# Optimization experiments

Measured on AMD Instinct MI355X. Metric: run time of the kernel, lower is better.

The kernel has to match this reference:

```python
import jax, jax.numpy as jnp
import numpy as np

S, B, H, V, U = 200, 1024, 128, 100000, 10000
LAMBDA_T = 0.1
LAMBDA_S = 1000.0
DAY = 86400.0


def setup_inputs() -> dict:
    key = jax.random.key(0)
    ks = jax.random.split(key, 14)
    x = jax.random.randint(ks[0], (S, B), 0, V)
    # monotone timestamps per sequence (gaps up to 1 hour)
    gaps = jax.random.uniform(ks[1], (S, B), minval=0.0, maxval=3600.0)
    t = jnp.cumsum(gaps, axis=0).astype(jnp.float32)
    # small spatial extent so exp(-1000*dist) doesn't fully underflow
    s = (jax.random.uniform(ks[2], (S, B, 2)) * 0.01).astype(jnp.float32)
    y_t = jax.random.uniform(ks[3], (S, B), dtype=jnp.float32)
    y_s = jax.random.uniform(ks[4], (S, B, 2), dtype=jnp.float32)
    h = jnp.zeros((B, H), dtype=jnp.float32)
    active_user = jax.random.randint(ks[5], (B,), 0, U)
    length = jax.random.randint(ks[6], (B,), 1, S + 1)
    W_enc = jax.random.normal(ks[7], (V, H), dtype=jnp.float32) * 0.02
    W_user = jax.random.normal(ks[8], (U, H), dtype=jnp.float32) * 0.02
    W_ih = jax.random.normal(ks[9], (H, H), dtype=jnp.float32) * 0.05
    W_hh = jax.random.normal(ks[10], (H, H), dtype=jnp.float32) * 0.05
    b_ih = jnp.zeros((H,), dtype=jnp.float32)
    b_hh = jnp.zeros((H,), dtype=jnp.float32)
    W_fc = jax.random.normal(ks[11], (V, 2 * H), dtype=jnp.float32) * 0.02
    b_fc = jnp.zeros((V,), dtype=jnp.float32)
    return {"x": x, "t": t, "s": s, "y_t": y_t, "y_s": y_s, "h": h,
            "active_user": active_user, "length": length,
            "W_enc": W_enc, "W_user": W_user, "W_ih": W_ih, "W_hh": W_hh,
            "b_ih": b_ih, "b_hh": b_hh, "W_fc": W_fc, "b_fc": b_fc}


def f_t(dt):
    return ((jnp.cos(dt * (2.0 * np.pi / DAY)) + 1.0) * 0.5) * jnp.exp(-(dt / DAY) * LAMBDA_T)


def f_s(ds):
    return jnp.exp(-ds * LAMBDA_S)


def reference(x, t, s, y_t, y_s, h, active_user, length,
              W_enc, W_user, W_ih, W_hh, b_ih, b_hh, W_fc, b_fc):
    seq_len, batch = x.shape
    x_emb = W_enc[x]  # [S,B,H]

    # vanilla tanh RNN over time (packing only affects padded steps, which are masked out below)
    def step(h_prev, x_t):
        h_new = jnp.tanh(x_t @ W_ih.T + b_ih + h_prev @ W_hh.T + b_hh)
        return h_new, h_new
    _, out = jax.lax.scan(step, h, x_emb)      # [S,B,H]
    out = out.transpose(1, 0, 2)               # [B,S,H]

    bidx = jnp.arange(batch)
    last = length - 1
    t_bt = t.T                                 # [B,S]
    s_bt = s.transpose(1, 0, 2)                # [B,S,2]
    t_last = t_bt[bidx, last]                  # [B]
    s_last = s_bt[bidx, last]                  # [B,2]

    dist_t = t_last[:, None] - t_bt                              # [B,S]
    dist_s = jnp.linalg.norm(s_last[:, None, :] - s_bt, axis=-1)  # [B,S]

    mask = jnp.arange(seq_len)[None, :] < length[:, None]        # [B,S] ragged mask
    w = jnp.where(mask, f_t(dist_t) * f_s(dist_s) + 1e-10, 0.0)  # [B,S]

    out_w = jnp.einsum('bs,bsh->bh', w, out) / jnp.sum(w, axis=1, keepdims=True)  # [B,H]

    p_u = W_user[active_user]                  # [B,H]
    out_pu = jnp.concatenate([out_w, p_u], axis=1)  # [B,2H]
    return out_pu @ W_fc.T + b_fc              # [B,V]
```

## Files before the change

kernel.cpp:

```cpp
#include <hip/hip_runtime.h>
#include <stdint.h>

#define S_LEN 200
#define BATCH 1024
#define HID   128
#define VOCAB 100000

typedef __attribute__((ext_vector_type(4))) float f32x4;
typedef __attribute__((ext_vector_type(8))) short bf16x8;

__device__ __forceinline__ unsigned short f2bf(float f) {
  union { float f; uint32_t u; } v; v.f = f;
  uint32_t u = v.u;
  uint32_t r = u + 0x7fffu + ((u >> 16) & 1u);
  return (unsigned short)(r >> 16);
}

__global__ __launch_bounds__(256) void k1_eprecomp(
    const float* __restrict__ Wenc, const float* __restrict__ Wih,
    const float* __restrict__ bih, const float* __restrict__ bhh,
    float* __restrict__ E) {
  __shared__ float Wlds[128][132];
  __shared__ float Alds[64][132];
  const int tid = threadIdx.x;
  const int v0 = blockIdx.x * 64;

  #pragma unroll
  for (int i = 0; i < 16; ++i) {
    int g = tid + i * 256;
    int row = g >> 5, c4 = g & 31;
    *(f32x4*)&Wlds[row][c4 * 4] = *(const f32x4*)&Wih[row * 128 + c4 * 4];
  }
  #pragma unroll
  for (int i = 0; i < 8; ++i) {
    int g = tid + i * 256;
    int row = g >> 5, c4 = g & 31;
    int v = v0 + row;
    *(f32x4*)&Alds[row][c4 * 4] =
        *(const f32x4*)&Wenc[(size_t)(v < VOCAB ? v : 0) * 128 + c4 * 4];
  }
  __syncthreads();

  const int jt = tid & 15, vt = tid >> 4;
  float acc[4][8];
  #pragma unroll
  for (int a = 0; a < 4; ++a)
    #pragma unroll
    for (int b = 0; b < 8; ++b) acc[a][b] = 0.f;

  for (int kk = 0; kk < 32; ++kk) {
    f32x4 av[4], wv[8];
    #pragma unroll
    for (int vv = 0; vv < 4; ++vv) av[vv] = *(const f32x4*)&Alds[vt + 16 * vv][kk * 4];
    #pragma unroll
    for (int jj = 0; jj < 8; ++jj) wv[jj] = *(const f32x4*)&Wlds[jt + 16 * jj][kk * 4];
    #pragma unroll
    for (int vv = 0; vv < 4; ++vv)
      #pragma unroll
      for (int jj = 0; jj < 8; ++jj)
        acc[vv][jj] += av[vv].x * wv[jj].x + av[vv].y * wv[jj].y +
                       av[vv].z * wv[jj].z + av[vv].w * wv[jj].w;
  }

  #pragma unroll
  for (int jj = 0; jj < 8; ++jj) {
    int j = jt + 16 * jj;
    float bias = bih[j] + bhh[j];
    #pragma unroll
    for (int vv = 0; vv < 4; ++vv) {
      int v = v0 + vt + 16 * vv;
      if (v < VOCAB) E[(size_t)v * 128 + j] = acc[vv][jj] + bias;
    }
  }
}

__global__ __launch_bounds__(256) void k1b_weights(
    const float* __restrict__ t, const float* __restrict__ s,
    const int* __restrict__ length, float* __restrict__ wbuf) {
  int idx = blockIdx.x * 256 + threadIdx.x;
  int ts = idx >> 10, b = idx & 1023;
  int len = length[b];
  float w = 0.f;
  if (ts < len) {
    int last = len - 1;
    float tl  = t[last * BATCH + b];
    float slx = s[(last * BATCH + b) * 2 + 0];
    float sly = s[(last * BATCH + b) * 2 + 1];
    float dt = tl - t[ts * BATCH + b];
    float dx = slx - s[(ts * BATCH + b) * 2 + 0];
    float dy = sly - s[(ts * BATCH + b) * 2 + 1];
    float ds = sqrtf(dx * dx + dy * dy);
    float ft = (__cosf(dt * 7.2722052166430399e-05f) + 1.f) * 0.5f *
               __expf(dt * -1.1574074074074073e-06f);
    float fs = __expf(-1000.f * ds);
    w = ft * fs + 1e-10f;
  }
  wbuf[idx] = w;
}

__global__ __launch_bounds__(256) void k2_rnn(
    const int* __restrict__ x, const float* __restrict__ E,
    const float* __restrict__ Whh, const float* __restrict__ h0,
    const float* __restrict__ wbuf,
    const int* __restrict__ active_user, const float* __restrict__ Wuser,
    float* __restrict__ A) {
  __shared__ float hlds[2][2][128];
  const int tid = threadIdx.x;
  const int lane = tid & 63, wv = tid >> 6;
  const int j = wv * 32 + (lane >> 1);
  const int kh = lane & 1;
  const int b0 = blockIdx.x * 2, b1 = b0 + 1;

  f32x4 Wr[16];
  const float* wrow = &Whh[j * 128 + kh * 64];
  #pragma unroll
  for (int i = 0; i < 16; ++i) Wr[i] = *(const f32x4*)&wrow[i * 4];

  { int bb = tid >> 7, jj = tid & 127;
    hlds[0][bb][jj] = h0[(b0 + bb) * 128 + jj]; }
  __syncthreads();

  float acc0 = 0.f, acc1 = 0.f, ws0 = 0.f, ws1 = 0.f;
  int xc0 = x[b0], xc1 = x[b1];
  int xn0 = x[1024 + b0], xn1 = x[1024 + b1];
  float ec0 = E[(size_t)xc0 * 128 + j], ec1 = E[(size_t)xc1 * 128 + j];
  float wc0 = wbuf[b0], wc1 = wbuf[b1];

  for (int t = 0; t < S_LEN; ++t) {
    int rb = t & 1, wb = rb ^ 1;
    int xf0 = 0, xf1 = 0;
    float en0 = 0.f, en1 = 0.f, wn0 = 0.f, wn1 = 0.f;
    if (t + 2 < S_LEN) { xf0 = x[(t + 2) * 1024 + b0]; xf1 = x[(t + 2) * 1024 + b1]; }
    if (t + 1 < S_LEN) {
      en0 = E[(size_t)xn0 * 128 + j]; en1 = E[(size_t)xn1 * 128 + j];
      wn0 = wbuf[(t + 1) * 1024 + b0]; wn1 = wbuf[(t + 1) * 1024 + b1];
    }
    float p0 = 0.f, p1 = 0.f;
    const float* h0p = &hlds[rb][0][kh * 64];
    const float* h1p = &hlds[rb][1][kh * 64];
    #pragma unroll
    for (int i = 0; i < 16; ++i) {
      f32x4 hv0 = *(const f32x4*)&h0p[i * 4];
      f32x4 hv1 = *(const f32x4*)&h1p[i * 4];
      p0 += Wr[i].x * hv0.x + Wr[i].y * hv0.y + Wr[i].z * hv0.z + Wr[i].w * hv0.w;
      p1 += Wr[i].x * hv1.x + Wr[i].y * hv1.y + Wr[i].z * hv1.z + Wr[i].w * hv1.w;
    }
    p0 += __shfl_xor(p0, 1, 64);
    p1 += __shfl_xor(p1, 1, 64);
    float hn0 = tanhf(p0 + ec0);
    float hn1 = tanhf(p1 + ec1);
    acc0 += wc0 * hn0; ws0 += wc0;
    acc1 += wc1 * hn1; ws1 += wc1;
    if (kh == 0) { hlds[wb][0][j] = hn0; hlds[wb][1][j] = hn1; }
    __syncthreads();
    xc0 = xn0; xc1 = xn1; xn0 = xf0; xn1 = xf1;
    ec0 = en0; ec1 = en1; wc0 = wn0; wc1 = wn1;
  }

  if (kh == 0) {
    A[b0 * 256 + j] = acc0 / ws0;
    A[b1 * 256 + j] = acc1 / ws1;
    int u0 = active_user[b0], u1 = active_user[b1];
    A[b0 * 256 + 128 + j] = Wuser[u0 * 128 + j];
    A[b1 * 256 + 128 + j] = Wuser[u1 * 128 + j];
  }
}

__global__ __launch_bounds__(256) void k3_gemm(
    const float* __restrict__ A, const float* __restrict__ Wfc,
    const float* __restrict__ bfc, float* __restrict__ out) {
  __shared__ unsigned short Alds[64 * 264];
  const int tid = threadIdx.x;
  const int nblk = blockIdx.x >> 4;
  const int mblk = blockIdx.x & 15;
  const int m0 = mblk * 64;
  const int v0 = nblk * 256;

  #pragma unroll
  for (int i = 0; i < 16; ++i) {
    int g = tid + i * 256;
    int row = g >> 6, c4 = g & 63;
    f32x4 a = *(const f32x4*)&A[(size_t)(m0 + row) * 256 + c4 * 4];
    uint2 pk;
    pk.x = (uint32_t)f2bf(a.x) | ((uint32_t)f2bf(a.y) << 16);
    pk.y = (uint32_t)f2bf(a.z) | ((uint32_t)f2bf(a.w) << 16);
    *(uint2*)((void*)&Alds[row * 264 + c4 * 4]) = pk;
  }
  __syncthreads();

  const int lane = tid & 63, wid = tid >> 6;
  const int lm = lane & 15, quad = lane >> 4;
  const int vbase = v0 + wid * 64;

  f32x4 acc[4][4];
  #pragma unroll
  for (int mt = 0; mt < 4; ++mt)
    #pragma unroll
    for (int nt = 0; nt < 4; ++nt) acc[mt][nt] = (f32x4){0.f, 0.f, 0.f, 0.f};

  const float* bptr[4];
  #pragma unroll
  for (int nt = 0; nt < 4; ++nt) {
    int v = vbase + nt * 16 + lm;
    int vc = v < VOCAB ? v : (VOCAB - 1);
    bptr[nt] = &Wfc[(size_t)vc * 256];
  }

  for (int kc = 0; kc < 8; ++kc) {
    const int k0 = kc * 32 + quad * 8;
    bf16x8 af[4], bfr[4];
    #pragma unroll
    for (int mt = 0; mt < 4; ++mt)
      af[mt] = *(const bf16x8*)&Alds[(mt * 16 + lm) * 264 + k0];
    #pragma unroll
    for (int nt = 0; nt < 4; ++nt) {
      f32x4 w0 = *(const f32x4*)&bptr[nt][k0];
      f32x4 w1 = *(const f32x4*)&bptr[nt][k0 + 4];
      bf16x8 b;
      b[0] = (short)f2bf(w0.x); b[1] = (short)f2bf(w0.y);
      b[2] = (short)f2bf(w0.z); b[3] = (short)f2bf(w0.w);
      b[4] = (short)f2bf(w1.x); b[5] = (short)f2bf(w1.y);
      b[6] = (short)f2bf(w1.z); b[7] = (short)f2bf(w1.w);
      bfr[nt] = b;
    }
    #pragma unroll
    for (int mt = 0; mt < 4; ++mt)
      #pragma unroll
      for (int nt = 0; nt < 4; ++nt)
        acc[mt][nt] = __builtin_amdgcn_mfma_f32_16x16x32_bf16(
            af[mt], bfr[nt], acc[mt][nt], 0, 0, 0);
  }

  #pragma unroll
  for (int nt = 0; nt < 4; ++nt) {
    int v = vbase + nt * 16 + lm;
    if (v >= VOCAB) continue;
    float bias = bfc[v];
    #pragma unroll
    for (int mt = 0; mt < 4; ++mt) {
      int row = m0 + mt * 16 + quad * 4;
      #pragma unroll
      for (int r = 0; r < 4; ++r)
        out[(size_t)(row + r) * VOCAB + v] = acc[mt][nt][r] + bias;
    }
  }
}

extern "C" void kernel_launch(void* const* d_in, const int* in_sizes, int n_in,
                              void* d_out, int out_size, void* d_ws, size_t ws_size,
                              hipStream_t stream) {
  const int*   x     = (const int*)d_in[0];
  const float* t     = (const float*)d_in[1];
  const float* s     = (const float*)d_in[2];
  const float* h0    = (const float*)d_in[5];
  const int*   au    = (const int*)d_in[6];
  const int*   len   = (const int*)d_in[7];
  const float* Wenc  = (const float*)d_in[8];
  const float* Wuser = (const float*)d_in[9];
  const float* Wih   = (const float*)d_in[10];
  const float* Whh   = (const float*)d_in[11];
  const float* bih   = (const float*)d_in[12];
  const float* bhh   = (const float*)d_in[13];
  const float* Wfc   = (const float*)d_in[14];
  const float* bfc   = (const float*)d_in[15];
  float* out = (float*)d_out;

  char* ws = (char*)d_ws;
  float* E    = (float*)(ws);
  float* wbuf = (float*)(ws + 51200000);
  float* A    = (float*)(ws + 52019200);

  k1_eprecomp<<<1563, 256, 0, stream>>>(Wenc, Wih, bih, bhh, E);
  k1b_weights<<<800, 256, 0, stream>>>(t, s, len, wbuf);
  k2_rnn<<<512, 256, 0, stream>>>(x, E, Whh, h0, wbuf, au, Wuser, A);
  k3_gemm<<<6256, 256, 0, stream>>>(A, Wfc, bfc, out);
}
```

Baseline: 1.074 ms.

## Pre-convert W_fc to bf16 once per call and swizzle GEMM A tile

Adds a kernel that converts W_fc to bf16 in workspace once per call, so each of the 16 M-blocks no longer re-reads and re-converts the fp32 weights. The RNN kernel now writes the activation matrix A directly as bf16. The GEMM stages A in LDS with an XOR swizzle instead of padding, and remaps block IDs so blocks sharing weight tiles are grouped. The bf16 path runs only if the workspace is large enough, otherwise it falls back to the fp32-conversion path. The cost is an extra full pass over W_fc (read fp32, write bf16) each call.

Measured after the change: 1.027 ms. 4.4% less time.

```diff
diff --git a/kernel.cpp b/kernel.cpp
--- a/kernel.cpp
+++ b/kernel.cpp
@@ -14,6 +14,19 @@
   uint32_t u = v.u;
   uint32_t r = u + 0x7fffu + ((u >> 16) & 1u);
   return (unsigned short)(r >> 16);
+}
+
+__global__ __launch_bounds__(256) void k0_wfc_bf16(
+    const float* __restrict__ Wfc, unsigned short* __restrict__ Wfcb) {
+  size_t i = ((size_t)blockIdx.x * 256 + threadIdx.x) * 8;
+  f32x4 a = *(const f32x4*)&Wfc[i];
+  f32x4 b = *(const f32x4*)&Wfc[i + 4];
+  uint4 pk;
+  pk.x = (uint32_t)f2bf(a.x) | ((uint32_t)f2bf(a.y) << 16);
+  pk.y = (uint32_t)f2bf(a.z) | ((uint32_t)f2bf(a.w) << 16);
+  pk.z = (uint32_t)f2bf(b.x) | ((uint32_t)f2bf(b.y) << 16);
+  pk.w = (uint32_t)f2bf(b.z) | ((uint32_t)f2bf(b.w) << 16);
+  *(uint4*)&Wfcb[i] = pk;
 }
 
 __global__ __launch_bounds__(256) void k1_eprecomp(
@@ -103,7 +116,7 @@
     const float* __restrict__ Whh, const float* __restrict__ h0,
     const float* __restrict__ wbuf,
     const int* __restrict__ active_user, const float* __restrict__ Wuser,
-    float* __restrict__ A) {
+    unsigned short* __restrict__ A) {
   __shared__ float hlds[2][2][128];
   const int tid = threadIdx.x;
   const int lane = tid & 63, wv = tid >> 6;
@@ -158,33 +171,35 @@
   }
 
   if (kh == 0) {
-    A[b0 * 256 + j] = acc0 / ws0;
-    A[b1 * 256 + j] = acc1 / ws1;
+    A[b0 * 256 + j] = f2bf(acc0 / ws0);
+    A[b1 * 256 + j] = f2bf(acc1 / ws1);
     int u0 = active_user[b0], u1 = active_user[b1];
-    A[b0 * 256 + 128 + j] = Wuser[u0 * 128 + j];
-    A[b1 * 256 + 128 + j] = Wuser[u1 * 128 + j];
-  }
-}
-
+    A[b0 * 256 + 128 + j] = f2bf(Wuser[u0 * 128 + j]);
+    A[b1 * 256 + 128 + j] = f2bf(Wuser[u1 * 128 + j]);
+  }
+}
+
+template <bool PRE>
 __global__ __launch_bounds__(256) void k3_gemm(
-    const float* __restrict__ A, const float* __restrict__ Wfc,
+    const unsigned short* __restrict__ Ab, const void* __restrict__ W,
     const float* __restrict__ bfc, float* __restrict__ out) {
-  __shared__ unsigned short Alds[64 * 264];
+  __shared__ unsigned short Alds[64 * 256];
   const int tid = threadIdx.x;
-  const int nblk = blockIdx.x >> 4;
-  const int mblk = blockIdx.x & 15;
+  const int bid = blockIdx.x;
+  const int linear = (bid & 7) * 782 + (bid >> 3);
+  const int nblk = linear >> 4;
+  const int mblk = linear & 15;
   const int m0 = mblk * 64;
   const int v0 = nblk * 256;
 
   #pragma unroll
-  for (int i = 0; i < 16; ++i) {
-    int g = tid + i * 256;
-    int row = g >> 6, c4 = g & 63;
-    f32x4 a = *(const f32x4*)&A[(size_t)(m0 + row) * 256 + c4 * 4];
-    uint2 pk;
-    pk.x = (uint32_t)f2bf(a.x) | ((uint32_t)f2bf(a.y) << 16);
-    pk.y = (uint32_t)f2bf(a.z) | ((uint32_t)f2bf(a.w) << 16);
-    *(uint2*)((void*)&Alds[row * 264 + c4 * 4]) = pk;
+  for (int i = 0; i < 8; ++i) {
+    int u = tid + i * 256;
+    int row = u >> 5, cu = u & 31;
+    uint32_t byte = (uint32_t)(row << 9) + (uint32_t)(cu << 4);
+    byte ^= (uint32_t)((row & 7) << 4);
+    uint4 val = *(const uint4*)&Ab[(size_t)(m0 + row) * 256 + cu * 8];
+    *(uint4*)((char*)Alds + byte) = val;
   }
   __syncthreads();
 
@@ -198,30 +213,42 @@
     #pragma unroll
     for (int nt = 0; nt < 4; ++nt) acc[mt][nt] = (f32x4){0.f, 0.f, 0.f, 0.f};
 
-  const float* bptr[4];
+  const char* bbase[4];
   #pragma unroll
   for (int nt = 0; nt < 4; ++nt) {
     int v = vbase + nt * 16 + lm;
-    int vc = v < VOCAB ? v : (VOCAB - 1);
-    bptr[nt] = &Wfc[(size_t)vc * 256];
+    size_t vc = (size_t)(v < VOCAB ? v : (VOCAB - 1));
+    if constexpr (PRE)
+      bbase[nt] = (const char*)((const unsigned short*)W + vc * 256);
+    else
+      bbase[nt] = (const char*)((const float*)W + vc * 256);
   }
 
   for (int kc = 0; kc < 8; ++kc) {
     const int k0 = kc * 32 + quad * 8;
     bf16x8 af[4], bfr[4];
     #pragma unroll
-    for (int mt = 0; mt < 4; ++mt)
-      af[mt] = *(const bf16x8*)&Alds[(mt * 16 + lm) * 264 + k0];
+    for (int mt = 0; mt < 4; ++mt) {
+      int row = mt * 16 + lm;
+      uint32_t byte = (uint32_t)(row << 9) + (uint32_t)(k0 << 1);
+      byte ^= (uint32_t)((row & 7) << 4);
+      af[mt] = *(const bf16x8*)((const char*)Alds + byte);
+    }
     #pragma unroll
     for (int nt = 0; nt < 4; ++nt) {
-      f32x4 w0 = *(const f32x4*)&bptr[nt][k0];
-      f32x4 w1 = *(const f32x4*)&bptr[nt][k0 + 4];
-      bf16x8 b;
-      b[0] = (short)f2bf(w0.x); b[1] = (short)f2bf(w0.y);
-      b[2] = (short)f2bf(w0.z); b[3] = (short)f2bf(w0.w);
-      b[4] = (short)f2bf(w1.x); b[5] = (short)f2bf(w1.y);
-      b[6] = (short)f2bf(w1.z); b[7] = (short)f2bf(w1.w);
-      bfr[nt] = b;
+      if constexpr (PRE) {
+        bfr[nt] = *(const bf16x8*)(bbase[nt] + (size_t)k0 * 2);
+      } else {
+        const float* bp = (const float*)bbase[nt];
+        f32x4 w0 = *(const f32x4*)&bp[k0];
+        f32x4 w1 = *(const f32x4*)&bp[k0 + 4];
+        bf16x8 b;
+        b[0] = (short)f2bf(w0.x); b[1] = (short)f2bf(w0.y);
+        b[2] = (short)f2bf(w0.z); b[3] = (short)f2bf(w0.w);
+        b[4] = (short)f2bf(w1.x); b[5] = (short)f2bf(w1.y);
+        b[6] = (short)f2bf(w1.z); b[7] = (short)f2bf(w1.w);
+        bfr[nt] = b;
+      }
     }
     #pragma unroll
     for (int mt = 0; mt < 4; ++mt)
@@ -266,12 +293,19 @@
   float* out = (float*)d_out;
 
   char* ws = (char*)d_ws;
-  float* E    = (float*)(ws);
-  float* wbuf = (float*)(ws + 51200000);
-  float* A    = (float*)(ws + 52019200);
-
+  float*          E    = (float*)(ws);
+  float*          wbuf = (float*)(ws + 51200000);
+  unsigned short* Ab   = (unsigned short*)(ws + 52019200);
+  unsigned short* Wfcb = (unsigned short*)(ws + 52543488);
+  const size_t need = 52543488ull + 51200000ull;
+  const bool pre = ws_size >= need;
+
+  if (pre) k0_wfc_bf16<<<12500, 256, 0, stream>>>(Wfc, Wfcb);
   k1_eprecomp<<<1563, 256, 0, stream>>>(Wenc, Wih, bih, bhh, E);
   k1b_weights<<<800, 256, 0, stream>>>(t, s, len, wbuf);
-  k2_rnn<<<512, 256, 0, stream>>>(x, E, Whh, h0, wbuf, au, Wuser, A);
-  k3_gemm<<<6256, 256, 0, stream>>>(A, Wfc, bfc, out);
-}
+  k2_rnn<<<512, 256, 0, stream>>>(x, E, Whh, h0, wbuf, au, Wuser, Ab);
+  if (pre)
+    k3_gemm<true><<<6256, 256, 0, stream>>>(Ab, (const void*)Wfcb, bfc, out);
+  else
+    k3_gemm<false><<<6256, 256, 0, stream>>>(Ab, (const void*)Wfc, bfc, out);
+}
```
